# Kernel optimization log

Hardware: AMD Instinct MI355X
Metric: run time of the kernel (lower is better)

Reference implementation:

```python
import jax, jax.numpy as jnp
import numpy as np

DATA_DIM = 128
UNITS = 512
LAYERS = 3
BATCH = 32
IN_STEPS = 1000   # int((T_input + 0.5*dt)//dt)
OUT_STEPS = 100   # int((T_output + 0.5*dt)//dt)


def setup_inputs() -> dict:
    key = jax.random.key(0)
    ks = jax.random.split(key, 16)
    d = {}
    d["x"] = jax.random.normal(ks[0], (BATCH, IN_STEPS, DATA_DIM), jnp.float32)
    in_dims = [DATA_DIM, UNITS, UNITS]
    i = 1
    for j in range(LAYERS):
        d[f"W{j}"] = jax.random.normal(ks[i], (in_dims[j], 3 * UNITS), jnp.float32) * 0.05; i += 1
        d[f"U{j}"] = jax.random.normal(ks[i], (UNITS, 3 * UNITS), jnp.float32) * 0.05; i += 1
        d[f"b{j}"] = jnp.zeros((2, 3 * UNITS), jnp.float32)
        d[f"s{j}"] = jax.random.normal(ks[i], (1, UNITS), jnp.float32); i += 1
    d["Wd"] = jax.random.normal(ks[i], (UNITS, DATA_DIM), jnp.float32) * 0.05
    d["bd"] = jnp.zeros((DATA_DIM,), jnp.float32)
    return d


def _gru_cell(x, h, W, U, b):
    # Keras GRUCell, reset_after=True (TF2 default)
    mx = x @ W + b[0]           # [B, 3U]
    mh = h @ U + b[1]           # [B, 3U]
    xz, xr, xh = jnp.split(mx, 3, axis=-1)
    hz, hr, hh = jnp.split(mh, 3, axis=-1)
    z = jax.nn.sigmoid(xz + hz)
    r = jax.nn.sigmoid(xr + hr)
    cand = jnp.tanh(xh + r * hh)
    return z * h + (1.0 - z) * cand


def reference(x, W0, U0, b0, s0, W1, U1, b1, s1, W2, U2, b2, s2, Wd, bd):
    params = [(W0, U0, b0), (W1, U1, b1), (W2, U2, b2)]
    B = x.shape[0]
    # learnable initial states, tiled over batch -> [L, B, U]
    h0 = jnp.stack([jnp.tile(s, (B, 1)) for s in (s0, s1, s2)])
    # model processes timesteps 0 .. in_steps-2 (last input step unused)
    xs = jnp.swapaxes(x[:, : IN_STEPS - 1, :], 0, 1)  # [T-1, B, D]

    def step(h, xt):
        hs = []
        inp = xt
        for j, (W, U, b) in enumerate(params):
            hj = _gru_cell(inp, h[j], W, U, b)
            hs.append(hj)
            inp = hj
        hn = jnp.stack(hs)  # [L, B, U]
        return hn, (inp, hn)

    _, (ys, hs) = jax.lax.scan(step, h0, xs)
    # outputs correspond to steps in_steps-out_steps-1 .. in_steps-2
    ys = ys[-OUT_STEPS:]   # [out_steps, B, U]
    hs = hs[-OUT_STEPS:]   # [out_steps, L, B, U]
    preds = ys @ Wd + bd   # [out_steps, B, D]
    predictions = jnp.swapaxes(preds, 0, 1)        # [B, out_steps, D]
    hidden = jnp.transpose(hs, (2, 0, 1, 3))       # [B, out_steps, L, U]
    return predictions, hidden
```

## Files before the change

kernel.cpp:

```cpp
#include <hip/hip_runtime.h>
#include <math.h>

#define B_   32
#define INS  1000
#define TS   999
#define D_   128
#define U_   512
#define G3   1536
#define OUTS 100
#define NB   208
#define NTICK 1002
#define NTHR 512

#define HBUF_OFF 0
#define HBUF_SZ  (2*3*512*32)
#define RING_OFF HBUF_SZ
#define RING_SZ  (4*1536*32)
#define BAR_OFF  (RING_OFF + RING_SZ)

#define W_CHK1  3080
#define W_CHK0  1544
#define XBUF_OFF 12288
#define PART_OFF 24640
#define SMEM_FLOATS 32384
#define PIDX3(q,g,c,e) ((q)*968 + ((g)*8+(c))*40 + (e))

#define WT_STORE(p, v) __hip_atomic_store((p), (v), __ATOMIC_RELAXED, __HIP_MEMORY_SCOPE_AGENT)
#define CG_LOAD(p)     __hip_atomic_load((p), __ATOMIC_RELAXED, __HIP_MEMORY_SCOPE_AGENT)

#define FMA12() \
  acc[0][0]=fmaf(av.x,w0,acc[0][0]); acc[0][1]=fmaf(av.y,w0,acc[0][1]); \
  acc[0][2]=fmaf(av.z,w0,acc[0][2]); acc[0][3]=fmaf(av.w,w0,acc[0][3]); \
  acc[1][0]=fmaf(av.x,w1,acc[1][0]); acc[1][1]=fmaf(av.y,w1,acc[1][1]); \
  acc[1][2]=fmaf(av.z,w1,acc[1][2]); acc[1][3]=fmaf(av.w,w1,acc[1][3]); \
  acc[2][0]=fmaf(av.x,w2,acc[2][0]); acc[2][1]=fmaf(av.y,w2,acc[2][1]); \
  acc[2][2]=fmaf(av.z,w2,acc[2][2]); acc[2][3]=fmaf(av.w,w2,acc[2][3]);

#define LD16(DST, PTR) { _Pragma("unroll") \
  for (int t_ = 0; t_ < 16; ++t_) DST[t_] = *(const float4*)((PTR) + t_*32); }

#define FMA16(BUF) { _Pragma("unroll") \
  for (int t_ = 0; t_ < 16; ++t_) { \
    const float w0 = wp[0], w1 = wp[1], w2 = wp[2]; \
    const float4 av = BUF[t_]; \
    FMA12(); \
    wp += 24; } }

__global__ void gru_init_kernel(const float* __restrict__ s0,
                                const float* __restrict__ s1,
                                const float* __restrict__ s2,
                                float* __restrict__ ws) {
  int g = blockIdx.x * 256 + threadIdx.x;
  if (g < 4096) { unsigned* bar = (unsigned*)(ws + BAR_OFF); bar[g] = 0u; }
  for (int i = g; i < 3 * 512 * 32; i += gridDim.x * 256) {
    int which = i / (512 * 32);
    int r = i - which * (512 * 32);
    int k = r >> 5, e = r & 31;
    int par = (which == 1) ? 1 : 0;
    const float* s = (which == 0) ? s0 : ((which == 1) ? s1 : s2);
    ws[HBUF_OFF + par * 49152 + which * 16384 + k * 32 + e] = s[k];
  }
}

__device__ __forceinline__ void gbar(unsigned* bar, unsigned ep, int bid) {
  __syncthreads();
  const int tid = threadIdx.x;
  if (tid == 0) WT_STORE(&bar[256 + bid * 16], ep);
  if (bid == 0) {
    if (tid < NB) {
      while (CG_LOAD(&bar[256 + tid * 16]) < ep) __builtin_amdgcn_s_sleep(1);
    }
    __syncthreads();
    if (tid == 0) WT_STORE(&bar[0], ep);
  }
  if (tid == 0) {
    while (CG_LOAD(&bar[0]) < ep) __builtin_amdgcn_s_sleep(1);
    __builtin_amdgcn_fence(__ATOMIC_ACQUIRE, "agent");
  }
  __syncthreads();
}

__global__ __launch_bounds__(NTHR, 1) void gru_persist(
    const float* __restrict__ x,
    const float* __restrict__ W0c, const float* __restrict__ U0c, const float* __restrict__ b0c,
    const float* __restrict__ W1c, const float* __restrict__ U1c, const float* __restrict__ b1c,
    const float* __restrict__ W2c, const float* __restrict__ U2c, const float* __restrict__ b2c,
    const float* __restrict__ Wd, const float* __restrict__ bd,
    float* __restrict__ out, float* __restrict__ ws)
{
  float* hbuf = ws + HBUF_OFF;
  float* ring = ws + RING_OFF;
  unsigned* bar = (unsigned*)(ws + BAR_OFF);
  float* pred_out = out;
  float* hid_out  = out + B_ * OUTS * D_;

  const int bid = blockIdx.x;
  const int tid = threadIdx.x;

  int role, rb;
  if      (bid < 16)  { role = -1; rb = bid; }
  else if (bid < 80)  { role = 0;  rb = bid - 16; }
  else if (bid < 144) { role = 1;  rb = bid - 80; }
  else                { role = 2;  rb = bid - 144; }

  __shared__ float smem[SMEM_FLOATS];
  float* part = smem + PART_OFF;

  const int eg  = tid & 7;
  const int c_l = (tid >> 3) & 7;
  const int q   = tid >> 6;
  const int cb  = (rb & 7) * 8 + (rb >> 3);
  const int c0  = cb * 8;
  const int rc = tid >> 5;
  const int re = tid & 31;
  const int xb0 = ((rb & 7) * 2 + (rb >> 3)) * 96;
  const int cg3 = (tid & 31) * 3;
  const int e0  = (tid >> 5) * 2;

  const float *Wj = nullptr, *Ujp = nullptr, *bj = nullptr;
  if      (role == 0) { Ujp = U0c; bj = b0c; }
  else if (role == 1) { Wj = W1c; Ujp = U1c; bj = b1c; }
  else if (role == 2) { Wj = W2c; Ujp = U2c; bj = b2c; }

  if (role < 0) {
    for (int idx = tid; idx < 128 * 96; idx += NTHR)
      smem[idx] = W0c[(idx / 96) * G3 + xb0 + (idx % 96)];
    for (int f = tid; f < 1024; f += NTHR) {
      int e = f >> 5, d4 = (f & 31) * 4;
      *(float4*)(smem + XBUF_OFF + e * 128 + d4) =
          *(const float4*)(x + e * (INS * D_) + d4);
    }
  } else {
    const int chunk = (role == 0) ? 64 : 128;
    const int chks  = (role == 0) ? W_CHK0 : W_CHK1;
    const int total = 8 * chunk * 24;
    for (int idx = tid; idx < total; idx += NTHR) {
      int qq = idx / (chunk * 24);
      int r  = idx - qq * (chunk * 24);
      int i  = r / 24;
      int cg = r - i * 24;
      int c  = cg / 3, g = cg - c * 3;
      const float* mat; int row;
      if (role == 0)      { mat = Ujp; row = qq * 64 + i; }
      else if (qq < 4)    { mat = Wj;  row = qq * 128 + i; }
      else                { mat = Ujp; row = (qq - 4) * 128 + i; }
      smem[qq * chks + (i * 8 + c) * 3 + g] = mat[row * G3 + g * 512 + c0 + c];
    }
  }
  float bz = 0.f, br = 0.f, b0h = 0.f, b1h = 0.f;
  if (role >= 0 && tid < 256) {
    const int cg2 = c0 + rc;
    bz  = bj[cg2] + bj[G3 + cg2];
    br  = bj[512 + cg2] + bj[G3 + 512 + cg2];
    b0h = bj[1024 + cg2];
    b1h = bj[G3 + 1024 + cg2];
  }
  __syncthreads();

  for (int T = 0; T < NTICK; ++T) {
    const int par_prev = (T + 1) & 1;
    const int par_cur  = T & 1;

    if (role < 0) {
      const int t = T;
      if (t < TS) {
        float4 xp0, xp1;
        const bool pf = (t + 1) < TS;
        if (pf) {
          int f0 = tid, f1 = tid + 512;
          xp0 = *(const float4*)(x + (f0 >> 5) * (INS * D_) + (t + 1) * D_ + (f0 & 31) * 4);
          xp1 = *(const float4*)(x + (f1 >> 5) * (INS * D_) + (t + 1) * D_ + (f1 & 31) * 4);
        }
        const float* xb = smem + XBUF_OFF + (t & 1) * 4096;
        float acc[3][2];
        #pragma unroll
        for (int c = 0; c < 3; ++c) { acc[c][0] = 0.f; acc[c][1] = 0.f; }
        #pragma unroll 4
        for (int k4 = 0; k4 < D_; k4 += 4) {
          float4 v0 = *(const float4*)(xb + e0 * 128 + k4);
          float4 v1 = *(const float4*)(xb + (e0 + 1) * 128 + k4);
          float xs0[4] = {v0.x, v0.y, v0.z, v0.w};
          float xs1[4] = {v1.x, v1.y, v1.z, v1.w};
          #pragma unroll
          for (int kk = 0; kk < 4; ++kk) {
            const float* wpx = smem + (k4 + kk) * 96 + cg3;
            float w0 = wpx[0], w1 = wpx[1], w2 = wpx[2];
            acc[0][0] = fmaf(xs0[kk], w0, acc[0][0]);
            acc[0][1] = fmaf(xs1[kk], w0, acc[0][1]);
            acc[1][0] = fmaf(xs0[kk], w1, acc[1][0]);
            acc[1][1] = fmaf(xs1[kk], w1, acc[1][1]);
            acc[2][0] = fmaf(xs0[kk], w2, acc[2][0]);
            acc[2][1] = fmaf(xs1[kk], w2, acc[2][1]);
          }
        }
        float* dst = ring + (t & 3) * (G3 * 32);
        #pragma unroll
        for (int c = 0; c < 3; ++c) {
          WT_STORE(dst + (xb0 + cg3 + c) * 32 + e0,     acc[c][0]);
          WT_STORE(dst + (xb0 + cg3 + c) * 32 + e0 + 1, acc[c][1]);
        }
        if (pf) {
          float* xw = smem + XBUF_OFF + ((t + 1) & 1) * 4096;
          int f0 = tid, f1 = tid + 512;
          *(float4*)(xw + (f0 >> 5) * 128 + (f0 & 31) * 4) = xp0;
          *(float4*)(xw + (f1 >> 5) * 128 + (f1 & 31) * 4) = xp1;
        }
      }
    } else {
      const int j = role;
      const int t = T - (j + 1);
      if (t >= 0 && t < TS) {
        const float* hprev_all = hbuf + par_prev * 49152;
        float xz = 0.f, xr2 = 0.f, xhv0 = 0.f, hp = 0.f;
        if (tid < 256) {
          const int cg2 = c0 + rc;
          hp = hprev_all[j * 16384 + cg2 * 32 + re];
          if (j == 0) {
            const float* r3 = ring + (t & 3) * (G3 * 32);
            xz   = r3[cg2 * 32 + re];
            xr2  = r3[(512 + cg2) * 32 + re];
            xhv0 = r3[(1024 + cg2) * 32 + re];
          }
        }

        float acc[3][4];
        #pragma unroll
        for (int g2 = 0; g2 < 3; ++g2)
          #pragma unroll
          for (int i2 = 0; i2 < 4; ++i2) acc[g2][i2] = 0.f;

        float4 bufA[16], bufB[16], bufC[16];
        if (j == 0) {
          const float* Ab = hprev_all + (q * 64) * 32 + eg * 4;
          const float* wp = smem + q * W_CHK0 + c_l * 3;
          LD16(bufA, Ab);        LD16(bufB, Ab + 512);
          LD16(bufC, Ab + 1024); FMA16(bufA);
          LD16(bufA, Ab + 1536); FMA16(bufB);
          FMA16(bufC);
          FMA16(bufA);
        } else {
          const int kb = (q & 3) * 128;
          const float* Ab = hprev_all + ((q < 4) ? (j - 1) : j) * 16384 + kb * 32 + eg * 4;
          const float* wp = smem + q * W_CHK1 + c_l * 3;
          LD16(bufA, Ab);        LD16(bufB, Ab + 512);
          LD16(bufC, Ab + 1024); FMA16(bufA);
          LD16(bufA, Ab + 1536); FMA16(bufB);
          LD16(bufB, Ab + 2048); FMA16(bufC);
          LD16(bufC, Ab + 2560); FMA16(bufA);
          LD16(bufA, Ab + 3072); FMA16(bufB);
          LD16(bufB, Ab + 3584); FMA16(bufC);
          FMA16(bufA);
          FMA16(bufB);
        }
        #pragma unroll
        for (int g2 = 0; g2 < 3; ++g2) {
          *(float4*)&part[PIDX3(q, g2, c_l, eg * 4)] =
              make_float4(acc[g2][0], acc[g2][1], acc[g2][2], acc[g2][3]);
        }
        __syncthreads();

        if (tid < 256) {
          float gz = 0.f, gr = 0.f, xh = 0.f, hh = 0.f;
          #pragma unroll
          for (int q2 = 0; q2 < 8; ++q2) {
            gz += part[PIDX3(q2, 0, rc, re)];
            gr += part[PIDX3(q2, 1, rc, re)];
            float v = part[PIDX3(q2, 2, rc, re)];
            if (j == 0)       hh += v;
            else if (q2 < 4)  xh += v;
            else              hh += v;
          }
          const int cg2 = c0 + rc;
          const float xhv = (j == 0) ? xhv0 : xh;
          const float zi = gz + xz + bz;
          const float ri = gr + xr2 + br;
          const float z = 1.f / (1.f + expf(-zi));
          const float r = 1.f / (1.f + expf(-ri));
          const float cand = tanhf((xhv + b0h) + r * (hh + b1h));
          const float hn = z * hp + (1.f - z) * cand;
          WT_STORE(&hbuf[par_cur * 49152 + j * 16384 + cg2 * 32 + re], hn);
          if (t >= TS - OUTS) {
            WT_STORE(&hid_out[((re * OUTS + (t - (TS - OUTS))) * 3 + j) * U_ + cg2], hn);
          }
        }
      }
    }
    gbar(bar, (unsigned)(T + 1), bid);
  }

  const int gt = bid * NTHR + tid;
  for (int o = gt; o < B_ * OUTS * D_; o += NB * NTHR) {
    int b  = o / (OUTS * D_);
    int r2 = o - b * (OUTS * D_);
    int s  = r2 >> 7;
    int dd = r2 & 127;
    const float* ys = hid_out + ((b * OUTS + s) * 3 + 2) * U_;
    float acc = bd[dd];
    #pragma unroll 4
    for (int k = 0; k < U_; k += 4) {
      float4 yv = *(const float4*)(ys + k);
      acc = fmaf(yv.x, Wd[(k    ) * D_ + dd], acc);
      acc = fmaf(yv.y, Wd[(k + 1) * D_ + dd], acc);
      acc = fmaf(yv.z, Wd[(k + 2) * D_ + dd], acc);
      acc = fmaf(yv.w, Wd[(k + 3) * D_ + dd], acc);
    }
    pred_out[o] = acc;
  }
}

extern "C" void kernel_launch(void* const* d_in, const int* in_sizes, int n_in,
                              void* d_out, int out_size, void* d_ws, size_t ws_size,
                              hipStream_t stream) {
  const float* x  = (const float*)d_in[0];
  const float* W0 = (const float*)d_in[1];
  const float* U0 = (const float*)d_in[2];
  const float* b0 = (const float*)d_in[3];
  const float* s0 = (const float*)d_in[4];
  const float* W1 = (const float*)d_in[5];
  const float* U1 = (const float*)d_in[6];
  const float* b1 = (const float*)d_in[7];
  const float* s1 = (const float*)d_in[8];
  const float* W2 = (const float*)d_in[9];
  const float* U2 = (const float*)d_in[10];
  const float* b2 = (const float*)d_in[11];
  const float* s2 = (const float*)d_in[12];
  const float* Wd = (const float*)d_in[13];
  const float* bd = (const float*)d_in[14];
  float* ws = (float*)d_ws;

  gru_init_kernel<<<192, 256, 0, stream>>>(s0, s1, s2, ws);
  gru_persist<<<NB, NTHR, 0, stream>>>(x, W0, U0, b0, W1, U1, b1,
                                       W2, U2, b2, Wd, bd, (float*)d_out, ws);
}
```

Before: 10.84 ms.

## Replace global grid barrier with per-block dependency flags and 4-deep hidden buffer

Removes the per-tick all-block barrier routed through block 0. Each block now publishes a per-step counter and waits only on the specific producer and consumer blocks it depends on: the same layer at t, the layer below at t+1, and ring-slot reuse at t-3. The hidden-state buffer grows from double to quadruple buffering so layers can drift up to a few steps apart, which lets the layers run as a pipeline without global lockstep. This adds more polling threads per block and more complex dependency logic, which raises the risk of races or deadlock.

```diff
diff --git a/kernel.cpp b/kernel.cpp
--- a/kernel.cpp
+++ b/kernel.cpp
@@ -9,11 +9,10 @@
 #define G3   1536
 #define OUTS 100
 #define NB   208
-#define NTICK 1002
 #define NTHR 512
 
 #define HBUF_OFF 0
-#define HBUF_SZ  (2*3*512*32)
+#define HBUF_SZ  (4*3*512*32)
 #define RING_OFF HBUF_SZ
 #define RING_SZ  (4*1536*32)
 #define BAR_OFF  (RING_OFF + RING_SZ)
@@ -56,28 +55,41 @@
     int which = i / (512 * 32);
     int r = i - which * (512 * 32);
     int k = r >> 5, e = r & 31;
-    int par = (which == 1) ? 1 : 0;
     const float* s = (which == 0) ? s0 : ((which == 1) ? s1 : s2);
-    ws[HBUF_OFF + par * 49152 + which * 16384 + k * 32 + e] = s[k];
-  }
-}
-
-__device__ __forceinline__ void gbar(unsigned* bar, unsigned ep, int bid) {
-  __syncthreads();
+    ws[HBUF_OFF + 3 * 49152 + which * 16384 + k * 32 + e] = s[k];
+  }
+}
+
+__device__ __forceinline__ void wait_deps(unsigned* slots, int role, int t) {
   const int tid = threadIdx.x;
-  if (tid == 0) WT_STORE(&bar[256 + bid * 16], ep);
-  if (bid == 0) {
-    if (tid < NB) {
-      while (CG_LOAD(&bar[256 + tid * 16]) < ep) __builtin_amdgcn_s_sleep(1);
-    }
+  const unsigned* p = nullptr; int tgt = 0;
+  if (role < 0) {
+    if (tid < 64)       { p = &slots[(0   + tid)       * 16]; tgt = t - 3; }
+  } else if (role == 0) {
+    if (tid < 64)       { p = &slots[(0   + tid)       * 16]; tgt = t;     }
+    else if (tid < 80)  { p = &slots[(192 + tid - 64)  * 16]; tgt = t + 1; }
+    else if (tid < 144) { p = &slots[(64  + tid - 80)  * 16]; tgt = t - 3; }
+  } else if (role == 1) {
+    if (tid < 64)       { p = &slots[(64  + tid)       * 16]; tgt = t;     }
+    else if (tid < 128) { p = &slots[(0   + tid - 64)  * 16]; tgt = t + 1; }
+    else if (tid < 192) { p = &slots[(128 + tid - 128) * 16]; tgt = t - 3; }
+  } else {
+    if (tid < 64)       { p = &slots[(128 + tid)       * 16]; tgt = t;     }
+    else if (tid < 128) { p = &slots[(64  + tid - 64)  * 16]; tgt = t + 1; }
+  }
+  if (p && tgt > 0) {
+    while ((int)CG_LOAD(p) < tgt) __builtin_amdgcn_s_sleep(1);
+  }
+  __syncthreads();
+  if (role >= 0) {
+    if (tid == 0) __builtin_amdgcn_fence(__ATOMIC_ACQUIRE, "agent");
     __syncthreads();
-    if (tid == 0) WT_STORE(&bar[0], ep);
-  }
-  if (tid == 0) {
-    while (CG_LOAD(&bar[0]) < ep) __builtin_amdgcn_s_sleep(1);
-    __builtin_amdgcn_fence(__ATOMIC_ACQUIRE, "agent");
-  }
-  __syncthreads();
+  }
+}
+
+__device__ __forceinline__ void publish(unsigned* slots, int sidx, int t) {
+  __syncthreads();
+  if (threadIdx.x == 0) WT_STORE(&slots[sidx * 16], (unsigned)(t + 1));
 }
 
 __global__ __launch_bounds__(NTHR, 1) void gru_persist(
@@ -90,7 +102,7 @@
 {
   float* hbuf = ws + HBUF_OFF;
   float* ring = ws + RING_OFF;
-  unsigned* bar = (unsigned*)(ws + BAR_OFF);
+  unsigned* slots = (unsigned*)(ws + BAR_OFF);
   float* pred_out = out;
   float* hid_out  = out + B_ * OUTS * D_;
 
@@ -102,6 +114,7 @@
   else if (bid < 80)  { role = 0;  rb = bid - 16; }
   else if (bid < 144) { role = 1;  rb = bid - 80; }
   else                { role = 2;  rb = bid - 144; }
+  const int sidx = (role < 0) ? (192 + rb) : (role * 64 + rb);
 
   __shared__ float smem[SMEM_FLOATS];
   float* part = smem + PART_OFF;
@@ -157,136 +170,138 @@
   }
   __syncthreads();
 
-  for (int T = 0; T < NTICK; ++T) {
-    const int par_prev = (T + 1) & 1;
-    const int par_cur  = T & 1;
+  for (int t = 0; t < TS; ++t) {
+    wait_deps(slots, role, t);
 
     if (role < 0) {
-      const int t = T;
-      if (t < TS) {
-        float4 xp0, xp1;
-        const bool pf = (t + 1) < TS;
-        if (pf) {
-          int f0 = tid, f1 = tid + 512;
-          xp0 = *(const float4*)(x + (f0 >> 5) * (INS * D_) + (t + 1) * D_ + (f0 & 31) * 4);
-          xp1 = *(const float4*)(x + (f1 >> 5) * (INS * D_) + (t + 1) * D_ + (f1 & 31) * 4);
+      float4 xp0, xp1;
+      const bool pf = (t + 1) < TS;
+      if (pf) {
+        int f0 = tid, f1 = tid + 512;
+        xp0 = *(const float4*)(x + (f0 >> 5) * (INS * D_) + (t + 1) * D_ + (f0 & 31) * 4);
+        xp1 = *(const float4*)(x + (f1 >> 5) * (INS * D_) + (t + 1) * D_ + (f1 & 31) * 4);
+      }
+      const float* xb = smem + XBUF_OFF + (t & 1) * 4096;
+      float acc[3][2];
+      #pragma unroll
+      for (int c = 0; c < 3; ++c) { acc[c][0] = 0.f; acc[c][1] = 0.f; }
+      #pragma unroll 4
+      for (int k4 = 0; k4 < D_; k4 += 4) {
+        float4 v0 = *(const float4*)(xb + e0 * 128 + k4);
+        float4 v1 = *(const float4*)(xb + (e0 + 1) * 128 + k4);
+        float xs0[4] = {v0.x, v0.y, v0.z, v0.w};
+        float xs1[4] = {v1.x, v1.y, v1.z, v1.w};
+        #pragma unroll
+        for (int kk = 0; kk < 4; ++kk) {
+          const float* wpx = smem + (k4 + kk) * 96 + cg3;
+          float w0 = wpx[0], w1 = wpx[1], w2 = wpx[2];
+          acc[0][0] = fmaf(xs0[kk], w0, acc[0][0]);
+          acc[0][1] = fmaf(xs1[kk], w0, acc[0][1]);
+          acc[1][0] = fmaf(xs0[kk], w1, acc[1][0]);
+          acc[1][1] = fmaf(xs1[kk], w1, acc[1][1]);
+          acc[2][0] = fmaf(xs0[kk], w2, acc[2][0]);
+          acc[2][1] = fmaf(xs1[kk], w2, acc[2][1]);
         }
-        const float* xb = smem + XBUF_OFF + (t & 1) * 4096;
-        float acc[3][2];
-        #pragma unroll
-        for (int c = 0; c < 3; ++c) { acc[c][0] = 0.f; acc[c][1] = 0.f; }
-        #pragma unroll 4
-        for (int k4 = 0; k4 < D_; k4 += 4) {
-          float4 v0 = *(const float4*)(xb + e0 * 128 + k4);
-          float4 v1 = *(const float4*)(xb + (e0 + 1) * 128 + k4);
-          float xs0[4] = {v0.x, v0.y, v0.z, v0.w};
-          float xs1[4] = {v1.x, v1.y, v1.z, v1.w};
-          #pragma unroll
-          for (int kk = 0; kk < 4; ++kk) {
-            const float* wpx = smem + (k4 + kk) * 96 + cg3;
-            float w0 = wpx[0], w1 = wpx[1], w2 = wpx[2];
-            acc[0][0] = fmaf(xs0[kk], w0, acc[0][0]);
-            acc[0][1] = fmaf(xs1[kk], w0, acc[0][1]);
-            acc[1][0] = fmaf(xs0[kk], w1, acc[1][0]);
-            acc[1][1] = fmaf(xs1[kk], w1, acc[1][1]);
-            acc[2][0] = fmaf(xs0[kk], w2, acc[2][0]);
-            acc[2][1] = fmaf(xs1[kk], w2, acc[2][1]);
-          }
-        }
-        float* dst = ring + (t & 3) * (G3 * 32);
-        #pragma unroll
-        for (int c = 0; c < 3; ++c) {
-          WT_STORE(dst + (xb0 + cg3 + c) * 32 + e0,     acc[c][0]);
-          WT_STORE(dst + (xb0 + cg3 + c) * 32 + e0 + 1, acc[c][1]);
-        }
-        if (pf) {
-          float* xw = smem + XBUF_OFF + ((t + 1) & 1) * 4096;
-          int f0 = tid, f1 = tid + 512;
-          *(float4*)(xw + (f0 >> 5) * 128 + (f0 & 31) * 4) = xp0;
-          *(float4*)(xw + (f1 >> 5) * 128 + (f1 & 31) * 4) = xp1;
-        }
+      }
+      float* dst = ring + (t & 3) * (G3 * 32);
+      #pragma unroll
+      for (int c = 0; c < 3; ++c) {
+        WT_STORE(dst + (xb0 + cg3 + c) * 32 + e0,     acc[c][0]);
+        WT_STORE(dst + (xb0 + cg3 + c) * 32 + e0 + 1, acc[c][1]);
+      }
+      if (pf) {
+        float* xw = smem + XBUF_OFF + ((t + 1) & 1) * 4096;
+        int f0 = tid, f1 = tid + 512;
+        *(float4*)(xw + (f0 >> 5) * 128 + (f0 & 31) * 4) = xp0;
+        *(float4*)(xw + (f1 >> 5) * 128 + (f1 & 31) * 4) = xp1;
       }
     } else {
       const int j = role;
-      const int t = T - (j + 1);
-      if (t >= 0 && t < TS) {
-        const float* hprev_all = hbuf + par_prev * 49152;
-        float xz = 0.f, xr2 = 0.f, xhv0 = 0.f, hp = 0.f;
-        if (tid < 256) {
-          const int cg2 = c0 + rc;
-          hp = hprev_all[j * 16384 + cg2 * 32 + re];
-          if (j == 0) {
-            const float* r3 = ring + (t & 3) * (G3 * 32);
-            xz   = r3[cg2 * 32 + re];
-            xr2  = r3[(512 + cg2) * 32 + re];
-            xhv0 = r3[(1024 + cg2) * 32 + re];
-          }
+      const float* hown = hbuf + ((t + 3) & 3) * 49152;
+      const float* hup  = hbuf + (t & 3) * 49152;
+      float xz = 0.f, xr2 = 0.f, xhv0 = 0.f, hp = 0.f;
+      if (tid < 256) {
+        const int cg2 = c0 + rc;
+        hp = hown[j * 16384 + cg2 * 32 + re];
+        if (j == 0) {
+          const float* r3 = ring + (t & 3) * (G3 * 32);
+          xz   = r3[cg2 * 32 + re];
+          xr2  = r3[(512 + cg2) * 32 + re];
+          xhv0 = r3[(1024 + cg2) * 32 + re];
         }
-
-        float acc[3][4];
+      }
+
+      float acc[3][4];
+      #pragma unroll
+      for (int g2 = 0; g2 < 3; ++g2)
         #pragma unroll
-        for (int g2 = 0; g2 < 3; ++g2)
-          #pragma unroll
-          for (int i2 = 0; i2 < 4; ++i2) acc[g2][i2] = 0.f;
-
-        float4 bufA[16], bufB[16], bufC[16];
-        if (j == 0) {
-          const float* Ab = hprev_all + (q * 64) * 32 + eg * 4;
-          const float* wp = smem + q * W_CHK0 + c_l * 3;
-          LD16(bufA, Ab);        LD16(bufB, Ab + 512);
-          LD16(bufC, Ab + 1024); FMA16(bufA);
-          LD16(bufA, Ab + 1536); FMA16(bufB);
-          FMA16(bufC);
-          FMA16(bufA);
-        } else {
-          const int kb = (q & 3) * 128;
-          const float* Ab = hprev_all + ((q < 4) ? (j - 1) : j) * 16384 + kb * 32 + eg * 4;
-          const float* wp = smem + q * W_CHK1 + c_l * 3;
-          LD16(bufA, Ab);        LD16(bufB, Ab + 512);
-          LD16(bufC, Ab + 1024); FMA16(bufA);
-          LD16(bufA, Ab + 1536); FMA16(bufB);
-          LD16(bufB, Ab + 2048); FMA16(bufC);
-          LD16(bufC, Ab + 2560); FMA16(bufA);
-          LD16(bufA, Ab + 3072); FMA16(bufB);
-          LD16(bufB, Ab + 3584); FMA16(bufC);
-          FMA16(bufA);
-          FMA16(bufB);
+        for (int i2 = 0; i2 < 4; ++i2) acc[g2][i2] = 0.f;
+
+      float4 bufA[16], bufB[16], bufC[16];
+      if (j == 0) {
+        const float* Ab = hown + (q * 64) * 32 + eg * 4;
+        const float* wp = smem + q * W_CHK0 + c_l * 3;
+        LD16(bufA, Ab);        LD16(bufB, Ab + 512);
+        LD16(bufC, Ab + 1024); FMA16(bufA);
+        LD16(bufA, Ab + 1536); FMA16(bufB);
+        FMA16(bufC);
+        FMA16(bufA);
+      } else {
+        const int kb = (q & 3) * 128;
+        const float* Ab = ((q < 4) ? (hup + (j - 1) * 16384) : (hown + j * 16384))
+                          + kb * 32 + eg * 4;
+        const float* wp = smem + q * W_CHK1 + c_l * 3;
+        LD16(bufA, Ab);        LD16(bufB, Ab + 512);
+        LD16(bufC, Ab + 1024); FMA16(bufA);
+        LD16(bufA, Ab + 1536); FMA16(bufB);
+        LD16(bufB, Ab + 2048); FMA16(bufC);
+        LD16(bufC, Ab + 2560); FMA16(bufA);
+        LD16(bufA, Ab + 3072); FMA16(bufB);
+        LD16(bufB, Ab + 3584); FMA16(bufC);
+        FMA16(bufA);
+        FMA16(bufB);
+      }
+      #pragma unroll
+      for (int g2 = 0; g2 < 3; ++g2) {
+        *(float4*)&part[PIDX3(q, g2, c_l, eg * 4)] =
+            make_float4(acc[g2][0], acc[g2][1], acc[g2][2], acc[g2][3]);
+      }
+      __syncthreads();
+
+      if (tid < 256) {
+        float gz = 0.f, gr = 0.f, xh = 0.f, hh = 0.f;
+        #pragma unroll
+        for (int q2 = 0; q2 < 8; ++q2) {
+          gz += part[PIDX3(q2, 0, rc, re)];
+          gr += part[PIDX3(q2, 1, rc, re)];
+          float v = part[PIDX3(q2, 2, rc, re)];
+          if (j == 0)       hh += v;
+          else if (q2 < 4)  xh += v;
+          else              hh += v;
         }
-        #pragma unroll
-        for (int g2 = 0; g2 < 3; ++g2) {
-          *(float4*)&part[PIDX3(q, g2, c_l, eg * 4)] =
-              make_float4(acc[g2][0], acc[g2][1], acc[g2][2], acc[g2][3]);
+        const int cg2 = c0 + rc;
+        const float xhv = (j == 0) ? xhv0 : xh;
+        const float zi = gz + xz + bz;
+        const float ri = gr + xr2 + br;
+        const float z = 1.f / (1.f + expf(-zi));
+        const float r = 1.f / (1.f + expf(-ri));
+        const float cand = tanhf((xhv + b0h) + r * (hh + b1h));
+        const float hn = z * hp + (1.f - z) * cand;
+        WT_STORE(&hbuf[(t & 3) * 49152 + j * 16384 + cg2 * 32 + re], hn);
+        if (t >= TS - OUTS) {
+          WT_STORE(&hid_out[((re * OUTS + (t - (TS - OUTS))) * 3 + j) * U_ + cg2], hn);
         }
-        __syncthreads();
-
-        if (tid < 256) {
-          float gz = 0.f, gr = 0.f, xh = 0.f, hh = 0.f;
-          #pragma unroll
-          for (int q2 = 0; q2 < 8; ++q2) {
-            gz += part[PIDX3(q2, 0, rc, re)];
-            gr += part[PIDX3(q2, 1, rc, re)];
-            float v = part[PIDX3(q2, 2, rc, re)];
-            if (j == 0)       hh += v;
-            else if (q2 < 4)  xh += v;
-            else              hh += v;
-          }
-          const int cg2 = c0 + rc;
-          const float xhv = (j == 0) ? xhv0 : xh;
-          const float zi = gz + xz + bz;
-          const float ri = gr + xr2 + br;
-          const float z = 1.f / (1.f + expf(-zi));
-          const float r = 1.f / (1.f + expf(-ri));
-          const float cand = tanhf((xhv + b0h) + r * (hh + b1h));
-          const float hn = z * hp + (1.f - z) * cand;
-          WT_STORE(&hbuf[par_cur * 49152 + j * 16384 + cg2 * 32 + re], hn);
-          if (t >= TS - OUTS) {
-            WT_STORE(&hid_out[((re * OUTS + (t - (TS - OUTS))) * 3 + j) * U_ + cg2], hn);
-          }
-        }
       }
     }
-    gbar(bar, (unsigned)(T + 1), bid);
-  }
+    publish(slots, sidx, t);
+  }
+
+  if (tid < 64) {
+    while ((int)CG_LOAD(&slots[(128 + tid) * 16]) < TS) __builtin_amdgcn_s_sleep(1);
+  }
+  __syncthreads();
+  if (tid == 0) __builtin_amdgcn_fence(__ATOMIC_ACQUIRE, "agent");
+  __syncthreads();
 
   const int gt = bid * NTHR + tid;
   for (int o = gt; o < B_ * OUTS * D_; o += NB * NTHR) {
```

After: 10.52 ms. -3.0%, faster.
